# Optimization experiments

Hardware: AMD Instinct MI355X
Metric: run time of the kernel (lower is better)

Reference implementation:

```python
import jax, jax.numpy as jnp
import numpy as np

E, K, H, I = 16, 4, 2048, 1024
B, S = 1, 2048


def setup_inputs() -> dict:
    key = jax.random.key(0)
    ks = jax.random.split(key, 5)
    scale_in = 1.0 / np.sqrt(H)
    scale_mid = 1.0 / np.sqrt(I)
    return {
        "x": jax.random.normal(ks[0], (B, S, H), dtype=jnp.float32),
        "gate_w": jax.random.normal(ks[1], (E, H), dtype=jnp.float32) * scale_in,
        "w1_gate": jax.random.normal(ks[2], (E, I, H), dtype=jnp.float32) * scale_in,
        "w1_up": jax.random.normal(ks[3], (E, I, H), dtype=jnp.float32) * scale_in,
        "w2": jax.random.normal(ks[4], (E, H, I), dtype=jnp.float32) * scale_mid,
        "topk": K,
    }


def reference(x, gate_w, w1_gate, w1_up, w2, topk):
    orig_shape = x.shape
    xt = x.reshape(-1, x.shape[-1])            # [T, H]
    T = xt.shape[0]
    n_exp = gate_w.shape[0]

    # Router: top-k logits, softmax over the selected k (as in the torch code).
    logits = xt @ gate_w.T                      # [T, E]
    topk_vals, topk_ids = jax.lax.top_k(logits, topk)
    topk_w = jax.nn.softmax(topk_vals, axis=-1)  # [T, K]

    # Dense per-token-per-expert combine weight; 0 for unselected experts.
    # Mathematically identical to the gather/scatter-add loop: unselected
    # experts contribute expert_out * 0.
    gate_dense = jnp.zeros((T, n_exp), dtype=xt.dtype)
    gate_dense = gate_dense.at[jnp.arange(T)[:, None], topk_ids].add(topk_w)

    # SwiGLU per expert (dense over experts; weights zero-out unused ones).
    g = jnp.einsum("th,eih->tei", xt, w1_gate)   # [T, E, I]
    u = jnp.einsum("th,eih->tei", xt, w1_up)     # [T, E, I]
    h = jax.nn.silu(g) * u                        # [T, E, I]
    out = jnp.einsum("tei,te,ehi->th", h, gate_dense, w2)  # [T, H]
    return out.reshape(orig_shape)
```

## Files before the change

kernel.cpp:

```cpp
#include <hip/hip_runtime.h>
#include <hip/hip_bf16.h>
#include <stdint.h>

#define NEXP 16
#define KSEL 4
#define HDIM 2048
#define IDIM 1024
#define TTOK 2048
#define MAXTILES 80
#define NTA 8
#define NTB 16
#define MAXBA (MAXTILES * NTA)
#define MAXBB (MAXTILES * NTB)
#define NCVT 1024
#define NW8 ((NEXP * IDIM * HDIM) / 8)

typedef __attribute__((ext_vector_type(8))) short bf16x8;
typedef __attribute__((ext_vector_type(4))) float f32x4;
typedef __attribute__((ext_vector_type(4))) unsigned int u32x4;
typedef unsigned int u32;

__device__ __forceinline__ uint32_t pack2(float a, float b) {
  __hip_bfloat162 h = __float22bfloat162_rn(float2{a, b});
  uint32_t u;
  __builtin_memcpy(&u, &h, 4);
  return u;
}
__device__ __forceinline__ ushort bf1(float a) {
  __hip_bfloat16 h = __float2bfloat16(a);
  ushort u;
  __builtin_memcpy(&u, &h, 2);
  return u;
}
__device__ __forceinline__ float bf2f(ushort u) {
  uint32_t v = (uint32_t)u << 16;
  float f;
  __builtin_memcpy(&f, &v, 4);
  return f;
}
__device__ __forceinline__ void gload16(const void* g, void* l) {
  __builtin_amdgcn_global_load_lds(
      (const __attribute__((address_space(1))) u32*)g,
      (__attribute__((address_space(3))) u32*)l, 16, 0, 0);
}
__device__ __forceinline__ int swzread(int row, int q) {
  return row * 32 + ((q ^ ((row >> 1) & 3)) << 3);
}
__device__ __forceinline__ void cvt_body(const float* __restrict__ src,
                                         ushort* __restrict__ dst,
                                         int blk, int nblk) {
  const int stride = nblk * 256;
  for (int i = blk * 256 + (int)threadIdx.x; i < NW8; i += stride) {
    f32x4 a = __builtin_nontemporal_load(((const f32x4*)src) + i * 2);
    f32x4 b = __builtin_nontemporal_load(((const f32x4*)src) + i * 2 + 1);
    uint4 t;
    t.x = pack2(a[0], a[1]); t.y = pack2(a[2], a[3]);
    t.z = pack2(b[0], b[1]); t.w = pack2(b[2], b[3]);
    ((uint4*)dst)[i] = t;
  }
}

__global__ __launch_bounds__(256) void router_kernel(
    const float* __restrict__ x, const float* __restrict__ gw,
    ushort* __restrict__ xb, int* __restrict__ topk_id,
    float* __restrict__ topk_w, const float* __restrict__ cvsrc,
    ushort* __restrict__ cvdst)
{
  if (blockIdx.x >= TTOK / 4) {
    cvt_body(cvsrc, cvdst, blockIdx.x - TTOK / 4, NCVT);
    return;
  }
  const int wid = threadIdx.x >> 6;
  const int lane = threadIdx.x & 63;
  const int t = blockIdx.x * 4 + wid;
  const float4* x4 = (const float4*)(x + (size_t)t * HDIM);
  const float4* gw4 = (const float4*)gw;
  float acc[NEXP];
#pragma unroll
  for (int e = 0; e < NEXP; ++e) acc[e] = 0.f;
#pragma unroll
  for (int i = 0; i < HDIM / 256; ++i) {
    const int idx = i * 64 + lane;
    float4 xv = x4[idx];
    uint2 xp;
    xp.x = pack2(xv.x, xv.y);
    xp.y = pack2(xv.z, xv.w);
    *(uint2*)(xb + (size_t)t * HDIM + idx * 4) = xp;
#pragma unroll
    for (int e = 0; e < NEXP; ++e) {
      float4 wv = gw4[e * (HDIM / 4) + idx];
      acc[e] += xv.x * wv.x + xv.y * wv.y + xv.z * wv.z + xv.w * wv.w;
    }
  }
#pragma unroll
  for (int e = 0; e < NEXP; ++e) {
#pragma unroll
    for (int off = 32; off >= 1; off >>= 1)
      acc[e] += __shfl_xor(acc[e], off);
  }
  if (lane == 0) {
    unsigned taken = 0;
    float vals[KSEL];
    int ids[KSEL];
#pragma unroll
    for (int k = 0; k < KSEL; ++k) {
      float bv = -3.4e38f; int bi = 0;
      for (int e = 0; e < NEXP; ++e)
        if (!((taken >> e) & 1u) && acc[e] > bv) { bv = acc[e]; bi = e; }
      taken |= 1u << bi; vals[k] = bv; ids[k] = bi;
    }
    float m = vals[0], s = 0.f, w[KSEL];
#pragma unroll
    for (int k = 0; k < KSEL; ++k) { w[k] = __expf(vals[k] - m); s += w[k]; }
    float is = 1.f / s;
#pragma unroll
    for (int k = 0; k < KSEL; ++k) {
      topk_id[t * KSEL + k] = ids[k];
      topk_w[t * KSEL + k] = w[k] * is;
    }
  }
}

__global__ __launch_bounds__(1024) void plan_scatter_kernel(
    const int* __restrict__ topk_id, int* __restrict__ counts,
    int* __restrict__ offsets, int* __restrict__ nWA, int* __restrict__ nWB,
    int* __restrict__ wlA, int* __restrict__ wlB,
    int* __restrict__ rowTok, int* __restrict__ inv)
{
  __shared__ int cnt[NEXP], off[NEXP], cur[NEXP], tiles[NEXP], pre[NEXP];
  const int tid = threadIdx.x;
  if (tid < NEXP) { cnt[tid] = 0; cur[tid] = 0; }
  __syncthreads();
  for (int i = tid; i < TTOK * KSEL; i += 1024)
    atomicAdd(&cnt[topk_id[i]], 1);
  __syncthreads();
  if (tid == 0) {
    int s = 0, p = 0;
    for (int e = 0; e < NEXP; ++e) {
      off[e] = s; s += cnt[e];
      tiles[e] = (cnt[e] + 127) >> 7;
      pre[e] = p; p += tiles[e];
    }
    *nWA = p * NTA;
    *nWB = p * NTB;
  }
  __syncthreads();
  if (tid < NEXP) {
    counts[tid] = cnt[tid];
    offsets[tid] = off[tid];
    const int e = tid, T = tiles[e];
    int idx = pre[e] * NTA;
    for (int nt = 0; nt < NTA; ++nt)
      for (int mt = 0; mt < T; ++mt)
        wlA[idx++] = (e << 12) | (nt << 6) | mt;
  } else if (tid < 2 * NEXP) {
    const int e = tid - NEXP, T = tiles[e];
    int idx = pre[e] * NTB;
    for (int nt = 0; nt < NTB; ++nt)
      for (int mt = 0; mt < T; ++mt)
        wlB[idx++] = (e << 12) | (nt << 6) | mt;
  }
  for (int i = tid; i < TTOK * KSEL; i += 1024) {
    const int e = topk_id[i];
    const int pos = atomicAdd(&cur[e], 1);
    const int row = off[e] + pos;
    rowTok[row] = i >> 2;
    inv[i] = row;
  }
}

__global__ __launch_bounds__(256) void gemmA_kernel(
    const ushort* __restrict__ xb, const ushort* __restrict__ wb,
    const int* __restrict__ rowTok, const int* __restrict__ counts,
    const int* __restrict__ offsets, const int* __restrict__ nW,
    const int* __restrict__ wl, ushort* __restrict__ outb,
    const float* __restrict__ cvsrc, ushort* __restrict__ cvdst)
{
  if (blockIdx.x >= MAXBA) {
    cvt_body(cvsrc, cvdst, blockIdx.x - MAXBA, NCVT);
    return;
  }
  const int nTot = *nW;
  const int L = (blockIdx.x & 7) * (MAXBA / 8) + (blockIdx.x >> 3);
  if (L >= nTot) return;
  const int w = wl[L];
  const int e = w >> 12, nt = (w >> 6) & 63, mt = w & 63;
  const int n_e = counts[e], rowbase = offsets[e];

  __shared__ ushort As[2][128 * 32];
  __shared__ ushort Bs[2][128 * 32];

  const int tid = threadIdx.x;
  const int r0 = tid >> 2;
  const int ck = tid & 3;
  const int sch = (ck ^ ((r0 >> 1) & 3)) << 3;

  const int ar0 = mt * 128 + r0, ar1 = ar0 + 64;
  const int tok0 = rowTok[rowbase + (ar0 < n_e ? ar0 : n_e - 1)];
  const int tok1 = rowTok[rowbase + (ar1 < n_e ? ar1 : n_e - 1)];
  const ushort* pA0 = xb + (size_t)tok0 * HDIM + sch;
  const ushort* pA1 = xb + (size_t)tok1 * HDIM + sch;
  const size_t wbase = (size_t)e * IDIM * HDIM;
  const ushort* pB0 = wb + wbase + (size_t)(nt * 128 + r0) * HDIM + sch;
  const ushort* pB1 = wb + wbase + (size_t)(nt * 128 + r0 + 64) * HDIM + sch;

  const int lane = tid & 63;
  const int wid = tid >> 6;
  const int wr = (wid >> 1) << 6;
  const int wc = (wid & 1) << 6;
  const int lr = lane & 15;
  const int q = lane >> 4;

  f32x4 acc[4][4];
#pragma unroll
  for (int i = 0; i < 4; ++i)
#pragma unroll
    for (int j = 0; j < 4; ++j) acc[i][j] = (f32x4){0.f, 0.f, 0.f, 0.f};

  auto STAGE = [&](int b) {
    gload16(pA0, &As[b][tid * 8]);
    gload16(pA1, &As[b][2048 + tid * 8]);
    gload16(pB0, &Bs[b][tid * 8]);
    gload16(pB1, &Bs[b][2048 + tid * 8]);
    pA0 += 32; pA1 += 32; pB0 += 32; pB1 += 32;
  };

  const int NTK = HDIM / 32;
  STAGE(0);
  __syncthreads();
  int buf = 0;
  for (int kt = 0; kt < NTK; ++kt) {
    if (kt + 1 < NTK) STAGE(buf ^ 1);
    bf16x8 af[4], bfr[4];
#pragma unroll
    for (int mi = 0; mi < 4; ++mi)
      af[mi] = *(const bf16x8*)&As[buf][swzread(wr + mi * 16 + lr, q)];
#pragma unroll
    for (int ni = 0; ni < 4; ++ni)
      bfr[ni] = *(const bf16x8*)&Bs[buf][swzread(wc + ni * 16 + lr, q)];
#pragma unroll
    for (int mi = 0; mi < 4; ++mi)
#pragma unroll
      for (int ni = 0; ni < 4; ++ni)
        acc[mi][ni] = __builtin_amdgcn_mfma_f32_16x16x32_bf16(af[mi], bfr[ni], acc[mi][ni], 0, 0, 0);
    __syncthreads();
    buf ^= 1;
  }

#pragma unroll
  for (int mi = 0; mi < 4; ++mi) {
#pragma unroll
    for (int ni = 0; ni < 4; ++ni) {
      const int col = nt * 128 + wc + ni * 16 + lr;
#pragma unroll
      for (int r = 0; r < 4; ++r) {
        const int mrow = mt * 128 + wr + mi * 16 + q * 4 + r;
        if (mrow < n_e)
          outb[(size_t)(rowbase + mrow) * IDIM + col] = bf1(acc[mi][ni][r]);
      }
    }
  }
}

__global__ __launch_bounds__(256) void gemmB_kernel(
    const ushort* __restrict__ hb, const ushort* __restrict__ wb,
    const int* __restrict__ counts, const int* __restrict__ offsets,
    const int* __restrict__ nW, const int* __restrict__ wl,
    ushort* __restrict__ po)
{
  const int nTot = *nW;
  const int L = (blockIdx.x & 7) * (MAXBB / 8) + (blockIdx.x >> 3);
  if (L >= nTot) return;
  const int w = wl[L];
  const int e = w >> 12, nt = (w >> 6) & 63, mt = w & 63;
  const int n_e = counts[e], rowbase = offsets[e];

  __shared__ ushort As[2][128 * 32];
  __shared__ ushort Bs[2][128 * 32];

  const int tid = threadIdx.x;
  const int r0 = tid >> 2;
  const int ck = tid & 3;
  const int sch = (ck ^ ((r0 >> 1) & 3)) << 3;

  const int ar0 = mt * 128 + r0, ar1 = ar0 + 64;
  const int g0 = rowbase + (ar0 < n_e ? ar0 : n_e - 1);
  const int g1 = rowbase + (ar1 < n_e ? ar1 : n_e - 1);
  const ushort* pA0 = hb + (size_t)g0 * IDIM + sch;
  const ushort* pA1 = hb + (size_t)g1 * IDIM + sch;
  const size_t wbase = (size_t)e * HDIM * IDIM;
  const ushort* pB0 = wb + wbase + (size_t)(nt * 128 + r0) * IDIM + sch;
  const ushort* pB1 = wb + wbase + (size_t)(nt * 128 + r0 + 64) * IDIM + sch;

  const int lane = tid & 63;
  const int wid = tid >> 6;
  const int wr = (wid >> 1) << 6;
  const int wc = (wid & 1) << 6;
  const int lr = lane & 15;
  const int q = lane >> 4;

  f32x4 acc[4][4];
#pragma unroll
  for (int i = 0; i < 4; ++i)
#pragma unroll
    for (int j = 0; j < 4; ++j) acc[i][j] = (f32x4){0.f, 0.f, 0.f, 0.f};

  auto STAGE = [&](int b) {
    gload16(pA0, &As[b][tid * 8]);
    gload16(pA1, &As[b][2048 + tid * 8]);
    gload16(pB0, &Bs[b][tid * 8]);
    gload16(pB1, &Bs[b][2048 + tid * 8]);
    pA0 += 32; pA1 += 32; pB0 += 32; pB1 += 32;
  };

  const int NTK = IDIM / 32;
  STAGE(0);
  __syncthreads();
  int buf = 0;
  for (int kt = 0; kt < NTK; ++kt) {
    if (kt + 1 < NTK) STAGE(buf ^ 1);
    bf16x8 af[4], bfr[4];
#pragma unroll
    for (int mi = 0; mi < 4; ++mi)
      af[mi] = *(const bf16x8*)&As[buf][swzread(wr + mi * 16 + lr, q)];
#pragma unroll
    for (int ni = 0; ni < 4; ++ni)
      bfr[ni] = *(const bf16x8*)&Bs[buf][swzread(wc + ni * 16 + lr, q)];
#pragma unroll
    for (int mi = 0; mi < 4; ++mi)
#pragma unroll
      for (int ni = 0; ni < 4; ++ni)
        acc[mi][ni] = __builtin_amdgcn_mfma_f32_16x16x32_bf16(af[mi], bfr[ni], acc[mi][ni], 0, 0, 0);
    __syncthreads();
    buf ^= 1;
  }

#pragma unroll
  for (int mi = 0; mi < 4; ++mi) {
#pragma unroll
    for (int ni = 0; ni < 4; ++ni) {
      const int col = nt * 128 + wc + ni * 16 + lr;
#pragma unroll
      for (int r = 0; r < 4; ++r) {
        const int mrow = mt * 128 + wr + mi * 16 + q * 4 + r;
        if (mrow < n_e)
          po[(size_t)(rowbase + mrow) * HDIM + col] = bf1(acc[mi][ni][r]);
      }
    }
  }
}

__global__ __launch_bounds__(256) void silu_kernel(
    const ushort* __restrict__ g, const ushort* __restrict__ u,
    ushort* __restrict__ h, int n8)
{
  const int stride = gridDim.x * 256;
  for (int i = blockIdx.x * 256 + threadIdx.x; i < n8; i += stride) {
    u32x4 gv = __builtin_nontemporal_load(((const u32x4*)g) + i);
    u32x4 uv = __builtin_nontemporal_load(((const u32x4*)u) + i);
    uint4 hv;
#pragma unroll
    for (int wd = 0; wd < 4; ++wd) {
      const uint32_t gw2 = gv[wd], uw2 = uv[wd];
      const float g0 = bf2f((ushort)(gw2 & 0xffff));
      const float g1 = bf2f((ushort)(gw2 >> 16));
      const float u0 = bf2f((ushort)(uw2 & 0xffff));
      const float u1 = bf2f((ushort)(uw2 >> 16));
      const float h0 = (g0 / (1.f + __expf(-g0))) * u0;
      const float h1 = (g1 / (1.f + __expf(-g1))) * u1;
      (&hv.x)[wd] = pack2(h0, h1);
    }
    ((uint4*)h)[i] = hv;
  }
}

__global__ __launch_bounds__(256) void combine_kernel(
    const ushort* __restrict__ po, const int* __restrict__ inv,
    const float* __restrict__ tw, float* __restrict__ out)
{
  const int t = blockIdx.x;
  const int r0 = inv[t * 4 + 0], r1 = inv[t * 4 + 1];
  const int r2 = inv[t * 4 + 2], r3 = inv[t * 4 + 3];
  const float w0 = tw[t * 4 + 0], w1 = tw[t * 4 + 1];
  const float w2v = tw[t * 4 + 2], w3 = tw[t * 4 + 3];
  const int i = threadIdx.x;
  uint4 v0 = *(const uint4*)(po + (size_t)r0 * HDIM + i * 8);
  uint4 v1 = *(const uint4*)(po + (size_t)r1 * HDIM + i * 8);
  uint4 v2 = *(const uint4*)(po + (size_t)r2 * HDIM + i * 8);
  uint4 v3 = *(const uint4*)(po + (size_t)r3 * HDIM + i * 8);
  float o[8];
#pragma unroll
  for (int w = 0; w < 4; ++w) {
    const uint32_t a = (&v0.x)[w], b = (&v1.x)[w], c = (&v2.x)[w], d = (&v3.x)[w];
    o[w * 2 + 0] = w0 * __builtin_bit_cast(float, a << 16) +
                   w1 * __builtin_bit_cast(float, b << 16) +
                   w2v * __builtin_bit_cast(float, c << 16) +
                   w3 * __builtin_bit_cast(float, d << 16);
    o[w * 2 + 1] = w0 * __builtin_bit_cast(float, a & 0xffff0000u) +
                   w1 * __builtin_bit_cast(float, b & 0xffff0000u) +
                   w2v * __builtin_bit_cast(float, c & 0xffff0000u) +
                   w3 * __builtin_bit_cast(float, d & 0xffff0000u);
  }
  float4* o4 = (float4*)(out + (size_t)t * HDIM + i * 8);
  o4[0] = (float4){o[0], o[1], o[2], o[3]};
  o4[1] = (float4){o[4], o[5], o[6], o[7]};
}

extern "C" void kernel_launch(void* const* d_in, const int* in_sizes, int n_in,
                              void* d_out, int out_size, void* d_ws, size_t ws_size,
                              hipStream_t stream) {
  const float* x   = (const float*)d_in[0];
  const float* gw  = (const float*)d_in[1];
  const float* w1g = (const float*)d_in[2];
  const float* w1u = (const float*)d_in[3];
  const float* w2  = (const float*)d_in[4];
  float* out = (float*)d_out;

  char* ws = (char*)d_ws;
  ushort* xb    = (ushort*)(ws + 0);
  ushort* wbufG = (ushort*)(ws + 8388608);
  ushort* wbufU = (ushort*)(ws + 75497472);
  ushort* wbuf2 = (ushort*)(ws + 142606336);
  ushort* gbuf  = (ushort*)(ws + 209715200);
  ushort* ubuf  = (ushort*)(ws + 226492416);
  ushort* hbuf  = (ushort*)(ws + 243269632);
  ushort* po    = (ushort*)(ws + 260046848);
  int*    tkid   = (int*)(ws + 293601280);
  float*  tkw    = (float*)(ws + 293601280 + 32768);
  int*    rowTok = (int*)(ws + 293601280 + 65536);
  int*    inv    = (int*)(ws + 293601280 + 98304);
  int*    ctrl   = (int*)(ws + 293732352);
  int* counts  = ctrl;
  int* offsets = ctrl + 32;
  int* nWA     = ctrl + 50;
  int* nWB     = ctrl + 51;
  int* wlA     = ctrl + 64;
  int* wlB     = ctrl + 64 + MAXBA;

  router_kernel<<<TTOK / 4 + NCVT, 256, 0, stream>>>(x, gw, xb, tkid, tkw,
                                                     w1g, wbufG);
  plan_scatter_kernel<<<1, 1024, 0, stream>>>(tkid, counts, offsets, nWA, nWB,
                                              wlA, wlB, rowTok, inv);
  gemmA_kernel<<<MAXBA + NCVT, 256, 0, stream>>>(xb, wbufG, rowTok, counts,
                                                 offsets, nWA, wlA, gbuf,
                                                 w1u, wbufU);
  gemmA_kernel<<<MAXBA + NCVT, 256, 0, stream>>>(xb, wbufU, rowTok, counts,
                                                 offsets, nWA, wlA, ubuf,
                                                 w2, wbuf2);
  silu_kernel<<<2048, 256, 0, stream>>>(gbuf, ubuf, hbuf, (TTOK * KSEL * IDIM) / 8);
  gemmB_kernel<<<MAXBB, 256, 0, stream>>>(hbuf, wbuf2, counts, offsets,
                                          nWB, wlB, po);
  combine_kernel<<<TTOK, 256, 0, stream>>>(po, inv, tkw, out);
}
```

Before: 350.0 us.

## Merge gate and up GEMM launches and move up-weight conversion to router

The gate and up projection GEMMs now run as one launch with twice the tile blocks, each half choosing its weight and output buffer. Because the up projection is now computed alongside the gate, the fp32-to-bf16 conversion of the up weights moves into the router launch, next to the gate-weight conversion. The w2 conversion stays in the merged GEMM launch. This drops one kernel launch and its tail, and gives the GPU more concurrent blocks per launch. The cost is a heavier router launch that now converts two weight tensors, and more cache pressure in the combined GEMM.

```diff
diff --git a/kernel.cpp b/kernel.cpp
--- a/kernel.cpp
+++ b/kernel.cpp
@@ -63,11 +63,16 @@
 __global__ __launch_bounds__(256) void router_kernel(
     const float* __restrict__ x, const float* __restrict__ gw,
     ushort* __restrict__ xb, int* __restrict__ topk_id,
-    float* __restrict__ topk_w, const float* __restrict__ cvsrc,
-    ushort* __restrict__ cvdst)
-{
+    float* __restrict__ topk_w,
+    const float* __restrict__ srcG, ushort* __restrict__ dstG,
+    const float* __restrict__ srcU, ushort* __restrict__ dstU)
+{
+  if (blockIdx.x >= TTOK / 4 + NCVT) {
+    cvt_body(srcU, dstU, blockIdx.x - (TTOK / 4 + NCVT), NCVT);
+    return;
+  }
   if (blockIdx.x >= TTOK / 4) {
-    cvt_body(cvsrc, cvdst, blockIdx.x - TTOK / 4, NCVT);
+    cvt_body(srcG, dstG, blockIdx.x - TTOK / 4, NCVT);
     return;
   }
   const int wid = threadIdx.x >> 6;
@@ -170,18 +175,26 @@
 }
 
 __global__ __launch_bounds__(256) void gemmA_kernel(
-    const ushort* __restrict__ xb, const ushort* __restrict__ wb,
+    const ushort* __restrict__ xb,
+    const ushort* __restrict__ wG, ushort* __restrict__ gbuf,
+    const ushort* __restrict__ wU, ushort* __restrict__ ubuf,
     const int* __restrict__ rowTok, const int* __restrict__ counts,
     const int* __restrict__ offsets, const int* __restrict__ nW,
-    const int* __restrict__ wl, ushort* __restrict__ outb,
+    const int* __restrict__ wl,
     const float* __restrict__ cvsrc, ushort* __restrict__ cvdst)
 {
-  if (blockIdx.x >= MAXBA) {
-    cvt_body(cvsrc, cvdst, blockIdx.x - MAXBA, NCVT);
+  int bid = blockIdx.x;
+  if (bid >= 2 * MAXBA) {
+    cvt_body(cvsrc, cvdst, bid - 2 * MAXBA, NCVT);
     return;
   }
+  const ushort* wb;
+  ushort* outb;
+  if (bid >= MAXBA) { wb = wU; outb = ubuf; bid -= MAXBA; }
+  else              { wb = wG; outb = gbuf; }
+
   const int nTot = *nW;
-  const int L = (blockIdx.x & 7) * (MAXBA / 8) + (blockIdx.x >> 3);
+  const int L = (bid & 7) * (MAXBA / 8) + (bid >> 3);
   if (L >= nTot) return;
   const int w = wl[L];
   const int e = w >> 12, nt = (w >> 6) & 63, mt = w & 63;
@@ -437,16 +450,13 @@
   int* wlA     = ctrl + 64;
   int* wlB     = ctrl + 64 + MAXBA;
 
-  router_kernel<<<TTOK / 4 + NCVT, 256, 0, stream>>>(x, gw, xb, tkid, tkw,
-                                                     w1g, wbufG);
+  router_kernel<<<TTOK / 4 + 2 * NCVT, 256, 0, stream>>>(
+      x, gw, xb, tkid, tkw, w1g, wbufG, w1u, wbufU);
   plan_scatter_kernel<<<1, 1024, 0, stream>>>(tkid, counts, offsets, nWA, nWB,
                                               wlA, wlB, rowTok, inv);
-  gemmA_kernel<<<MAXBA + NCVT, 256, 0, stream>>>(xb, wbufG, rowTok, counts,
-                                                 offsets, nWA, wlA, gbuf,
-                                                 w1u, wbufU);
-  gemmA_kernel<<<MAXBA + NCVT, 256, 0, stream>>>(xb, wbufU, rowTok, counts,
-                                                 offsets, nWA, wlA, ubuf,
-                                                 w2, wbuf2);
+  gemmA_kernel<<<2 * MAXBA + NCVT, 256, 0, stream>>>(
+      xb, wbufG, gbuf, wbufU, ubuf, rowTok, counts, offsets, nWA, wlA,
+      w2, wbuf2);
   silu_kernel<<<2048, 256, 0, stream>>>(gbuf, ubuf, hbuf, (TTOK * KSEL * IDIM) / 8);
   gemmB_kernel<<<MAXBB, 256, 0, stream>>>(hbuf, wbuf2, counts, offsets,
                                           nWB, wlB, po);
```

After: 327.0 us. 6.6% less time.
